# Performance work log

Measured on AMD Instinct MI355X. Metric: run time of the kernel, lower is better.

## Reference

```python
import jax, jax.numpy as jnp
import numpy as np

CHUNK = 2048  # mirrors torch.chunk(pc, len(pc)//2048) with N a multiple of 2048


def _half(src, ref):
    """Faithful to the original: for each chunk of `src`, compute the
    [M, chunk] squared-distance matrix against `ref` and take min over the
    chunk axis (dim 1), yielding an M-vector per chunk; concatenate.
    Result shape: [num_chunks * M]."""
    chunks = src.reshape(-1, CHUNK, src.shape[-1])  # [num_chunks, CHUNK, 3]

    def per_chunk(chunk):
        diff = ref[:, None, :] - chunk[None, :, :]          # [M, CHUNK, 3]
        d = jnp.square(jnp.sqrt(jnp.sum(diff * diff, -1)))  # norm(...)**2
        return jnp.min(d, axis=1)                           # [M]

    return jax.lax.map(per_chunk, chunks).reshape(-1)


def setup_inputs() -> dict:
    key = jax.random.key(0)
    k1, k2 = jax.random.split(key)
    output_pc = jax.random.normal(k1, (1, 16384, 3), dtype=jnp.float32)
    gt_pc = jax.random.normal(k2, (1, 16384, 3), dtype=jnp.float32)
    return {"output_pc": output_pc, "gt_pc": gt_pc}


def reference(output_pc, gt_pc):
    pc1 = jnp.squeeze(output_pc)  # [N, 3]
    pc2 = jnp.squeeze(gt_pc)      # [M, 3]
    dist1 = _half(pc1, pc2)       # [ (N//CHUNK) * M ]
    dist2 = _half(pc2, pc1)       # [ (M//CHUNK) * N ]
    return jnp.mean(dist1) + jnp.mean(dist2)
```

## Files before the change

### kernel.cpp

```cpp
#include <hip/hip_runtime.h>
#include <float.h>

#define CHUNK 2048
#define SUB   2048
#define MBLK  128

typedef __attribute__((ext_vector_type(8)))  short short8;
typedef __attribute__((ext_vector_type(16))) float f32x16;

static __device__ __forceinline__ unsigned short f2bf(float f) {
    unsigned u = __float_as_uint(f);
    return (unsigned short)((u + 0x7FFFu + ((u >> 16) & 1u)) >> 16);
}
static __device__ __forceinline__ float bf2f(unsigned short s) {
    return __uint_as_float(((unsigned)s) << 16);
}

__global__ void pack_kernel(const float* __restrict__ p1,
                            const float* __restrict__ p2, int n1, int n2,
                            unsigned short* __restrict__ Arec,
                            unsigned short* __restrict__ Brec)
{
    int i = blockIdx.x * blockDim.x + threadIdx.x;
    if (i >= n1 + n2) return;
    const bool isA = (i < n1);
    const float* s = isA ? p1 : p2;
    const int j = isA ? i : i - n1;
    float x = s[3 * j + 0], y = s[3 * j + 1], z = s[3 * j + 2];

    unsigned short r[16];
    if (isA) {
        unsigned short hx = f2bf(x), hy = f2bf(y), hz = f2bf(z);
        unsigned short lx = f2bf(x - bf2f(hx)), ly = f2bf(y - bf2f(hy)),
                       lz = f2bf(z - bf2f(hz));
        float sp = fmaf(x, x, fmaf(y, y, z * z));
        unsigned short sh = f2bf(sp), sl = f2bf(sp - bf2f(sh));
        r[0]=hx; r[1]=hy; r[2]=hz;  r[3]=lx; r[4]=ly; r[5]=lz;
        r[6]=hx; r[7]=hy; r[8]=hz;  r[9]=lx; r[10]=ly; r[11]=lz;
        r[12]=sh; r[13]=sl; r[14]=0x3F80; r[15]=0x3F80;
        unsigned short* dst = Arec + (size_t)j * 16;
#pragma unroll
        for (int t = 0; t < 16; ++t) dst[t] = r[t];
    } else {
        float ux = -2.0f * x, uy = -2.0f * y, uz = -2.0f * z;
        unsigned short hx = f2bf(ux), hy = f2bf(uy), hz = f2bf(uz);
        unsigned short lx = f2bf(ux - bf2f(hx)), ly = f2bf(uy - bf2f(hy)),
                       lz = f2bf(uz - bf2f(hz));
        float sq = fmaf(x, x, fmaf(y, y, z * z));
        unsigned short sh = f2bf(sq), sl = f2bf(sq - bf2f(sh));
        r[0]=hx; r[1]=hy; r[2]=hz;  r[3]=hx; r[4]=hy; r[5]=hz;
        r[6]=lx; r[7]=ly; r[8]=lz;  r[9]=lx; r[10]=ly; r[11]=lz;
        r[12]=0x3F80; r[13]=0x3F80; r[14]=sh; r[15]=sl;
        unsigned short* dst = Brec + (size_t)j * 16;
#pragma unroll
        for (int t = 0; t < 16; ++t) dst[t] = r[t];
    }
}

static __device__ __forceinline__ float tourney16(float rm[16], int l31)
{
#pragma unroll
    for (int r = 0; r < 8; ++r) {
        float lo = fminf(rm[r],     __shfl_xor(rm[r],     16));
        float hi = fminf(rm[r + 8], __shfl_xor(rm[r + 8], 16));
        rm[r] = (l31 & 16) ? hi : lo;
    }
#pragma unroll
    for (int r = 0; r < 4; ++r) {
        float lo = fminf(rm[r],     __shfl_xor(rm[r],     8));
        float hi = fminf(rm[r + 4], __shfl_xor(rm[r + 4], 8));
        rm[r] = (l31 & 8) ? hi : lo;
    }
#pragma unroll
    for (int r = 0; r < 2; ++r) {
        float lo = fminf(rm[r],     __shfl_xor(rm[r],     4));
        float hi = fminf(rm[r + 2], __shfl_xor(rm[r + 2], 4));
        rm[r] = (l31 & 4) ? hi : lo;
    }
    {
        float lo = fminf(rm[0], __shfl_xor(rm[0], 2));
        float hi = fminf(rm[1], __shfl_xor(rm[1], 2));
        rm[0] = (l31 & 2) ? hi : lo;
    }
    return fminf(rm[0], __shfl_xor(rm[0], 1));
}

__global__ __launch_bounds__(256, 8)
void chamfer_mfma(const unsigned short* __restrict__ Arec,
                  const unsigned short* __restrict__ Brec,
                  float* __restrict__ part2, float* __restrict__ part1,
                  int n1, int n2)
{
    const int dir = blockIdx.z;
    const unsigned short* __restrict__ Ap = dir ? Brec : Arec;
    const unsigned short* __restrict__ Bp = dir ? Arec : Brec;
    float* __restrict__ part = dir ? part1 : part2;
    const int rows_n = dir ? n2 : n1;
    const int cols_n = dir ? n1 : n2;

    const int tid  = threadIdx.x;
    const int g    = blockIdx.x;
    const int yb   = blockIdx.y;
    if (g * MBLK >= rows_n || yb * SUB >= cols_n) return;

    const int lane = tid & 63;
    const int w    = tid >> 6;
    const int half = lane >> 5;
    const int l31  = lane & 31;

    const int rA = g * MBLK + w * 32 + l31;
    short8 aA = *(const short8*)(Ap + (size_t)rA * 16 + half * 8);

    const unsigned short* bp =
        Bp + (size_t)(yb * SUB + l31) * 16 + half * 8;

    const f32x16 z16 = {0,0,0,0, 0,0,0,0, 0,0,0,0, 0,0,0,0};
    float rm[16];
#pragma unroll
    for (int r = 0; r < 16; ++r) rm[r] = FLT_MAX;

    const int NT = SUB / 32;
    for (int t = 0; t < NT; ++t) {
        short8 b = *(const short8*)(bp + (size_t)t * 512);
        f32x16 d = __builtin_amdgcn_mfma_f32_32x32x16_bf16(aA, b, z16, 0, 0, 0);
#pragma unroll
        for (int r = 0; r < 16; ++r) rm[r] = fminf(rm[r], d[r]);
    }

    float v = tourney16(rm, l31);
    if ((l31 & 1) == 0) {
        int r = (l31 >> 1) & 15;
        int rowl = (r & 3) + 8 * (r >> 2) + 4 * half;
        int grow = g * MBLK + w * 32 + rowl;
        part[(size_t)yb * rows_n + grow] = fmaxf(v, 0.0f);
    }
}

__global__ __launch_bounds__(256)
void pass2_kernel(const float* __restrict__ part2,
                  const float* __restrict__ part1, float* __restrict__ out,
                  int n1, int n2, int total2, int total1, float s2, float s1)
{
    __shared__ float wred[4];
    const int gpc = CHUNK / SUB;
    const int n = total2 + total1;
    float s = 0.0f;
    for (int idx = blockIdx.x * 256 + threadIdx.x; idx < n;
         idx += gridDim.x * 256) {
        float m = FLT_MAX;
        if (idx < total2) {
            int cc  = idx / n1;
            int row = idx - cc * n1;
#pragma unroll
            for (int t = 0; t < gpc; ++t)
                m = fminf(m, part2[(size_t)(cc * gpc + t) * n1 + row]);
            s += fmaxf(m, 0.0f) * s2;
        } else {
            int i1  = idx - total2;
            int c1  = i1 / n2;
            int col = i1 - c1 * n2;
#pragma unroll
            for (int t = 0; t < gpc; ++t)
                m = fminf(m, part1[(size_t)(c1 * gpc + t) * n2 + col]);
            s += fmaxf(m, 0.0f) * s1;
        }
    }
#pragma unroll
    for (int off = 32; off > 0; off >>= 1) s += __shfl_down(s, off);
    const int lane = threadIdx.x & 63, w = threadIdx.x >> 6;
    if (lane == 0) wred[w] = s;
    __syncthreads();
    if (threadIdx.x == 0)
        atomicAdd(out, wred[0] + wred[1] + wred[2] + wred[3]);
}

#define FB_RPT  2
#define FB_TILE (256 * FB_RPT)
__global__ __launch_bounds__(256, 2)
void chamfer_valu(const float* __restrict__ p1, const float* __restrict__ p2,
                  int n1, int n2, float* __restrict__ out)
{
    __shared__ float4 q[CHUNK];
    __shared__ float wsum[4];
    const int dir = blockIdx.z;
    const float* __restrict__ src = dir ? p2 : p1;
    const float* __restrict__ ref = dir ? p1 : p2;
    const int nsrc = dir ? n2 : n1;
    const int m    = dir ? n1 : n2;
    const int nchunks = nsrc / CHUNK;
    const int c = blockIdx.y;
    const int tile0 = blockIdx.x * FB_TILE;
    if (c >= nchunks || tile0 >= m) return;
    const float scale = 1.0f / ((float)nchunks * (float)m);
    const float* __restrict__ chunk = src + (size_t)c * CHUNK * 3;
    for (int k = threadIdx.x; k < CHUNK; k += 256) {
        float x = chunk[3*k], y = chunk[3*k+1], z = chunk[3*k+2];
        q[k] = make_float4(x, y, z, fmaf(x, x, fmaf(y, y, z * z)));
    }
    __syncthreads();
    float px[FB_RPT], py[FB_RPT], pz[FB_RPT], sp[FB_RPT], mna[FB_RPT], mnb[FB_RPT];
    bool valid[FB_RPT];
#pragma unroll
    for (int r = 0; r < FB_RPT; ++r) {
        int j = tile0 + threadIdx.x + r * 256;
        valid[r] = (j < m);
        int jj = valid[r] ? j : 0;
        float x = ref[3*jj], y = ref[3*jj+1], z = ref[3*jj+2];
        px[r] = -2.0f*x; py[r] = -2.0f*y; pz[r] = -2.0f*z;
        sp[r] = fmaf(x, x, fmaf(y, y, z * z));
        mna[r] = FLT_MAX; mnb[r] = FLT_MAX;
    }
#pragma unroll 2
    for (int k = 0; k < CHUNK; k += 2) {
        float4 qa = q[k], qb = q[k+1];
#pragma unroll
        for (int r = 0; r < FB_RPT; ++r) {
            mna[r] = fminf(mna[r], fmaf(px[r], qa.x, fmaf(py[r], qa.y, fmaf(pz[r], qa.z, qa.w))));
            mnb[r] = fminf(mnb[r], fmaf(px[r], qb.x, fmaf(py[r], qb.y, fmaf(pz[r], qb.z, qb.w))));
        }
    }
    float sum = 0.0f;
#pragma unroll
    for (int r = 0; r < FB_RPT; ++r)
        if (valid[r]) sum += fmaxf(fminf(mna[r], mnb[r]) + sp[r], 0.0f);
#pragma unroll
    for (int off = 32; off > 0; off >>= 1) sum += __shfl_down(sum, off);
    if ((threadIdx.x & 63) == 0) wsum[threadIdx.x >> 6] = sum;
    __syncthreads();
    if (threadIdx.x == 0)
        atomicAdd(out, (wsum[0]+wsum[1]+wsum[2]+wsum[3]) * scale);
}

extern "C" void kernel_launch(void* const* d_in, const int* in_sizes, int n_in,
                              void* d_out, int out_size, void* d_ws, size_t ws_size,
                              hipStream_t stream)
{
    const float* p1 = (const float*)d_in[0];
    const float* p2 = (const float*)d_in[1];
    float* out = (float*)d_out;
    const int n1 = in_sizes[0] / 3;
    const int n2 = in_sizes[1] / 3;

    const int nc1 = n1 / CHUNK, nc2 = n2 / CHUNK;
    const int nyb2 = n2 / SUB;
    const int nyb1 = n1 / SUB;

    unsigned short* Arec = (unsigned short*)d_ws;
    unsigned short* Brec = Arec + (size_t)n1 * 16;
    float* part2 = (float*)(Brec + (size_t)n2 * 16);
    float* part1 = part2 + (size_t)nyb2 * n1;
    const size_t need = (size_t)n1 * 32 + (size_t)n2 * 32 +
                        ((size_t)nyb2 * n1 + (size_t)nyb1 * n2) * 4;

    const bool shapes_ok = (n1 % CHUNK == 0) && (n2 % CHUNK == 0) &&
                           (n1 % MBLK == 0) && (n2 % MBLK == 0) &&
                           (n1 % SUB == 0) && (n2 % SUB == 0);

    if (shapes_ok && ws_size >= need) {
        pack_kernel<<<(n1 + n2 + 255) / 256, 256, 0, stream>>>(
            p1, p2, n1, n2, Arec, Brec);
        const int gx = max(n1, n2) / MBLK;
        const int gy = max(n1, n2) / SUB;
        dim3 grid(gx, gy, 2);
        chamfer_mfma<<<grid, 256, 0, stream>>>(Arec, Brec, part2, part1, n1, n2);
        const int total2 = nc2 * n1, total1 = nc1 * n2;
        pass2_kernel<<<512, 256, 0, stream>>>(
            part2, part1, out, n1, n2, total2, total1,
            1.0f / ((float)nc2 * (float)n1), 1.0f / ((float)nc1 * (float)n2));
    } else {
        const int t1 = (n2 + FB_TILE - 1) / FB_TILE;
        const int t2 = (n1 + FB_TILE - 1) / FB_TILE;
        dim3 grid(max(t1, t2), max(nc1, nc2), 2);
        chamfer_valu<<<grid, 256, 0, stream>>>(p1, p2, n1, n2, out);
    }
}
```

Baseline: 88.10 us.

## Fuse final reduction into MFMA kernel and stage B tiles through LDS

After: 94.68 us. +7.5%, slower.

```diff
diff --git a/kernel.cpp b/kernel.cpp
--- a/kernel.cpp
+++ b/kernel.cpp
@@ -4,6 +4,8 @@
 #define CHUNK 2048
 #define SUB   2048
 #define MBLK  128
+#define GRP   256
+#define NGRP  (SUB / GRP)
 
 typedef __attribute__((ext_vector_type(8)))  short short8;
 typedef __attribute__((ext_vector_type(16))) float f32x16;
@@ -14,6 +16,12 @@
 }
 static __device__ __forceinline__ float bf2f(unsigned short s) {
     return __uint_as_float(((unsigned)s) << 16);
+}
+
+static __device__ __forceinline__ void gld16(const void* g, void* l) {
+    __builtin_amdgcn_global_load_lds(
+        (const __attribute__((address_space(1))) void*)g,
+        (__attribute__((address_space(3))) void*)l, 16, 0, 0);
 }
 
 __global__ void pack_kernel(const float* __restrict__ p1,
@@ -88,13 +96,16 @@
 __global__ __launch_bounds__(256, 8)
 void chamfer_mfma(const unsigned short* __restrict__ Arec,
                   const unsigned short* __restrict__ Brec,
-                  float* __restrict__ part2, float* __restrict__ part1,
-                  int n1, int n2)
-{
+                  float* __restrict__ out,
+                  int n1, int n2, float s2, float s1)
+{
+    __shared__ alignas(16) unsigned short sb[2][GRP * 16];
+    __shared__ float wred[4];
+
     const int dir = blockIdx.z;
     const unsigned short* __restrict__ Ap = dir ? Brec : Arec;
     const unsigned short* __restrict__ Bp = dir ? Arec : Brec;
-    float* __restrict__ part = dir ? part1 : part2;
+    const float scale = dir ? s1 : s2;
     const int rows_n = dir ? n2 : n1;
     const int cols_n = dir ? n1 : n2;
 
@@ -111,67 +122,48 @@
     const int rA = g * MBLK + w * 32 + l31;
     short8 aA = *(const short8*)(Ap + (size_t)rA * 16 + half * 8);
 
-    const unsigned short* bp =
-        Bp + (size_t)(yb * SUB + l31) * 16 + half * 8;
-
+    const char* Bbytes = (const char*)(Bp + (size_t)(yb * SUB) * 16);
+
+    float rm[16];
+#pragma unroll
+    for (int r = 0; r < 16; ++r) rm[r] = FLT_MAX;
     const f32x16 z16 = {0,0,0,0, 0,0,0,0, 0,0,0,0, 0,0,0,0};
-    float rm[16];
-#pragma unroll
-    for (int r = 0; r < 16; ++r) rm[r] = FLT_MAX;
-
-    const int NT = SUB / 32;
-    for (int t = 0; t < NT; ++t) {
-        short8 b = *(const short8*)(bp + (size_t)t * 512);
-        f32x16 d = __builtin_amdgcn_mfma_f32_32x32x16_bf16(aA, b, z16, 0, 0, 0);
-#pragma unroll
-        for (int r = 0; r < 16; ++r) rm[r] = fminf(rm[r], d[r]);
+
+    {
+        const char* gp = Bbytes + tid * 16;
+        char* lp = (char*)&sb[0][0] + w * 1024;
+        gld16(gp, lp);
+        gld16(gp + 4096, lp + 4096);
+    }
+    __syncthreads();
+
+    for (int gr = 0; gr < NGRP; ++gr) {
+        const int cur = gr & 1;
+        if (gr + 1 < NGRP) {
+            const char* gp = Bbytes + (size_t)(gr + 1) * 8192 + tid * 16;
+            char* lp = (char*)&sb[cur ^ 1][0] + w * 1024;
+            gld16(gp, lp);
+            gld16(gp + 4096, lp + 4096);
+        }
+        const unsigned short* lb = &sb[cur][l31 * 16 + half * 8];
+#pragma unroll
+        for (int tt = 0; tt < GRP / 32; ++tt) {
+            short8 b = *(const short8*)(lb + tt * 512);
+            f32x16 d = __builtin_amdgcn_mfma_f32_32x32x16_bf16(aA, b, z16, 0, 0, 0);
+#pragma unroll
+            for (int r = 0; r < 16; ++r) rm[r] = fminf(rm[r], d[r]);
+        }
+        __syncthreads();
     }
 
     float v = tourney16(rm, l31);
-    if ((l31 & 1) == 0) {
-        int r = (l31 >> 1) & 15;
-        int rowl = (r & 3) + 8 * (r >> 2) + 4 * half;
-        int grow = g * MBLK + w * 32 + rowl;
-        part[(size_t)yb * rows_n + grow] = fmaxf(v, 0.0f);
-    }
-}
-
-__global__ __launch_bounds__(256)
-void pass2_kernel(const float* __restrict__ part2,
-                  const float* __restrict__ part1, float* __restrict__ out,
-                  int n1, int n2, int total2, int total1, float s2, float s1)
-{
-    __shared__ float wred[4];
-    const int gpc = CHUNK / SUB;
-    const int n = total2 + total1;
-    float s = 0.0f;
-    for (int idx = blockIdx.x * 256 + threadIdx.x; idx < n;
-         idx += gridDim.x * 256) {
-        float m = FLT_MAX;
-        if (idx < total2) {
-            int cc  = idx / n1;
-            int row = idx - cc * n1;
-#pragma unroll
-            for (int t = 0; t < gpc; ++t)
-                m = fminf(m, part2[(size_t)(cc * gpc + t) * n1 + row]);
-            s += fmaxf(m, 0.0f) * s2;
-        } else {
-            int i1  = idx - total2;
-            int c1  = i1 / n2;
-            int col = i1 - c1 * n2;
-#pragma unroll
-            for (int t = 0; t < gpc; ++t)
-                m = fminf(m, part1[(size_t)(c1 * gpc + t) * n2 + col]);
-            s += fmaxf(m, 0.0f) * s1;
-        }
-    }
-#pragma unroll
-    for (int off = 32; off > 0; off >>= 1) s += __shfl_down(s, off);
-    const int lane = threadIdx.x & 63, w = threadIdx.x >> 6;
-    if (lane == 0) wred[w] = s;
-    __syncthreads();
-    if (threadIdx.x == 0)
-        atomicAdd(out, wred[0] + wred[1] + wred[2] + wred[3]);
+    float c = ((l31 & 1) == 0) ? fmaxf(v, 0.0f) : 0.0f;
+#pragma unroll
+    for (int off = 32; off > 0; off >>= 1) c += __shfl_down(c, off);
+    if (lane == 0) wred[w] = c;
+    __syncthreads();
+    if (tid == 0)
+        atomicAdd(out, (wred[0] + wred[1] + wred[2] + wred[3]) * scale);
 }
 
 #define FB_RPT  2
@@ -242,15 +234,10 @@
     const int n2 = in_sizes[1] / 3;
 
     const int nc1 = n1 / CHUNK, nc2 = n2 / CHUNK;
-    const int nyb2 = n2 / SUB;
-    const int nyb1 = n1 / SUB;
 
     unsigned short* Arec = (unsigned short*)d_ws;
     unsigned short* Brec = Arec + (size_t)n1 * 16;
-    float* part2 = (float*)(Brec + (size_t)n2 * 16);
-    float* part1 = part2 + (size_t)nyb2 * n1;
-    const size_t need = (size_t)n1 * 32 + (size_t)n2 * 32 +
-                        ((size_t)nyb2 * n1 + (size_t)nyb1 * n2) * 4;
+    const size_t need = (size_t)(n1 + n2) * 32;
 
     const bool shapes_ok = (n1 % CHUNK == 0) && (n2 % CHUNK == 0) &&
                            (n1 % MBLK == 0) && (n2 % MBLK == 0) &&
@@ -262,10 +249,8 @@
         const int gx = max(n1, n2) / MBLK;
         const int gy = max(n1, n2) / SUB;
         dim3 grid(gx, gy, 2);
-        chamfer_mfma<<<grid, 256, 0, stream>>>(Arec, Brec, part2, part1, n1, n2);
-        const int total2 = nc2 * n1, total1 = nc1 * n2;
-        pass2_kernel<<<512, 256, 0, stream>>>(
-            part2, part1, out, n1, n2, total2, total1,
+        chamfer_mfma<<<grid, 256, 0, stream>>>(
+            Arec, Brec, out, n1, n2,
             1.0f / ((float)nc2 * (float)n1), 1.0f / ((float)nc1 * (float)n2));
     } else {
         const int t1 = (n2 + FB_TILE - 1) / FB_TILE;
```
